# Kernel optimization log

Hardware: AMD Instinct MI355X
Metric: run time of the kernel (lower is better)

Reference implementation:

```python
import jax, jax.numpy as jnp
import numpy as np

THETA = 10000.0

def apply_rope(x, positions):
    # x: [B, H, S, d_k], positions: [S] int
    d_k = x.shape[-1]
    inv_freq = THETA ** (-jnp.arange(0, d_k, 2, dtype=jnp.float32) / d_k)  # [d_k/2]
    ang = positions.astype(jnp.float32)[:, None] * inv_freq[None, :]        # [S, d_k/2]
    cos, sin = jnp.cos(ang), jnp.sin(ang)
    x_even = x[..., 0::2]
    x_odd = x[..., 1::2]
    r_even = x_even * cos - x_odd * sin
    r_odd = x_even * sin + x_odd * cos
    # interleave back
    return jnp.stack([r_even, r_odd], axis=-1).reshape(x.shape)

def setup_inputs() -> dict:
    key = jax.random.key(0)
    k1, k2, k3 = jax.random.split(key, 3)
    B, S, D = 2, 2048, 1024
    x = jax.random.normal(k1, (B, S, D), dtype=jnp.float32)
    token_positions = jnp.arange(S, dtype=jnp.int32)
    W_qkv = jax.random.normal(k2, (3 * D, D), dtype=jnp.float32) * 0.02
    W_o = jax.random.normal(k3, (D, D), dtype=jnp.float32) * 0.02
    return {"x": x, "token_positions": token_positions, "W_qkv": W_qkv, "W_o": W_o}

def reference(x, token_positions, W_qkv, W_o):
    B, S, D = x.shape
    H = 16
    d_k = D // H
    qkv = jnp.einsum('bsd,ed->bse', x, W_qkv)           # [B, S, 3D]
    q, k, v = jnp.split(qkv, 3, axis=-1)
    def to_heads(t):
        return t.reshape(B, S, H, d_k).transpose(0, 2, 1, 3)  # [B, H, S, d_k]
    hq, hk, hv = to_heads(q), to_heads(k), to_heads(v)
    hq = apply_rope(hq, token_positions)
    hk = apply_rope(hk, token_positions)
    scale = d_k ** -0.5
    scores = jnp.einsum('bhqd,bhkd->bhqk', hq, hk) * scale  # [B, H, S, S]
    causal = jnp.tril(jnp.ones((S, S), dtype=bool))
    scores = jnp.where(causal, scores, -jnp.inf)
    attn = jax.nn.softmax(scores, axis=-1)
    out = jnp.einsum('bhqk,bhkd->bhqd', attn, hv)           # [B, H, S, d_k]
    out = out.transpose(0, 2, 1, 3).reshape(B, S, D)
    return jnp.einsum('bsd,ed->bse', out, W_o)
```

## Files before the change

### kernel.cpp

```cpp
#include <hip/hip_runtime.h>
#include <math.h>

typedef short short8 __attribute__((ext_vector_type(8)));
typedef float f32x4 __attribute__((ext_vector_type(4)));
typedef unsigned int u32x2 __attribute__((ext_vector_type(2)));

typedef __attribute__((address_space(1))) const void* as1p;
typedef __attribute__((address_space(3))) void* as3p;

__device__ __forceinline__ unsigned short f2bf(float f) {
    unsigned int u = __float_as_uint(f);
    u += 0x7fffu + ((u >> 16) & 1u);
    return (unsigned short)(u >> 16);
}

__global__ void cvt_all_bf16(const float* __restrict__ x,
                             const float* __restrict__ wqkv,
                             const float* __restrict__ wo,
                             unsigned short* __restrict__ xb,
                             unsigned short* __restrict__ wqkvb,
                             unsigned short* __restrict__ wob) {
    int i = blockIdx.x * blockDim.x + threadIdx.x;
    const float* src;
    unsigned short* dst;
    int off;
    if (i < 1048576)       { src = x;    dst = xb;    off = i; }
    else if (i < 1835008)  { src = wqkv; dst = wqkvb; off = i - 1048576; }
    else                   { src = wo;   dst = wob;   off = i - 1835008; }
    float4 v = ((const float4*)src)[off];
    ushort4 o = make_ushort4(f2bf(v.x), f2bf(v.y), f2bf(v.z), f2bf(v.w));
    ((ushort4*)dst)[off] = o;
}

template <int RF, int NTX, bool BF16_OUT, bool DO_ROPE>
__global__ __launch_bounds__(256) void gemm_nt_mfma(
    const unsigned short* __restrict__ A, const unsigned short* __restrict__ B,
    void* __restrict__ Cv, const int* __restrict__ pos, int N, int K) {
    constexpr int BM = RF * 32;
    __shared__ unsigned short As[BM * 32];
    __shared__ unsigned short Bs[128 * 32];
    const int tid = threadIdx.x;
    const int wave = tid >> 6, lane = tid & 63;
    const int L = blockIdx.x;
    const int xcd = L & 7, idx = L >> 3;
    const int nt_ = xcd * NTX + idx % NTX;
    const int mt  = idx / NTX;
    const int m0 = mt * BM, n0 = nt_ << 7;
    const int wr = ((wave >> 1) & 1) * (RF * 16);
    const int wc = (wave & 1) << 6;

    const int r0 = tid >> 2;
    const int ko = (((tid & 3) ^ ((r0 >> 1) & 3)) << 3);
    const unsigned short* Ap0 = A + (size_t)(m0 + r0) * K + ko;
    const unsigned short* Ap1 = A + (size_t)(m0 + (RF == 4 ? 64 : 0) + r0) * K + ko;
    const unsigned short* Bp0 = B + (size_t)(n0 + r0) * K + ko;
    const unsigned short* Bp1 = B + (size_t)(n0 + 64 + r0) * K + ko;

    f32x4 acc[RF][4] = {};
    const int lro = lane & 15;
    const int cs = ((lane >> 4) ^ ((lro >> 1) & 3)) << 3;

    for (int k0 = 0; k0 < K; k0 += 32) {
        __syncthreads();
        __builtin_amdgcn_global_load_lds((as1p)(Ap0 + k0), (as3p)(As + tid * 8), 16, 0, 0);
        if constexpr (RF == 4)
            __builtin_amdgcn_global_load_lds((as1p)(Ap1 + k0), (as3p)(As + (256 + tid) * 8), 16, 0, 0);
        __builtin_amdgcn_global_load_lds((as1p)(Bp0 + k0), (as3p)(Bs + tid * 8), 16, 0, 0);
        __builtin_amdgcn_global_load_lds((as1p)(Bp1 + k0), (as3p)(Bs + (256 + tid) * 8), 16, 0, 0);
        __syncthreads();

        short8 af[RF], bfr[4];
        #pragma unroll
        for (int i = 0; i < RF; i++) af[i] = *(const short8*)&As[(wr + i * 16 + lro) * 32 + cs];
        #pragma unroll
        for (int j = 0; j < 4; j++) bfr[j] = *(const short8*)&Bs[(wc + j * 16 + lro) * 32 + cs];
        #pragma unroll
        for (int i = 0; i < RF; i++)
            #pragma unroll
            for (int j = 0; j < 4; j++)
                acc[i][j] = __builtin_amdgcn_mfma_f32_16x16x32_bf16(af[i], bfr[j], acc[i][j], 0, 0, 0);
    }

    const int row_b = m0 + wr + ((lane >> 4) << 2);
    const int col_b = n0 + wc + lro;

    if constexpr (DO_ROPE) {
        const int sec = (n0 + wc) >> 10;
        if (sec < 2) {
            const float qs = (sec == 0) ? 0.18033688011112042f : 1.0f;
            const float sgn = (lane & 1) ? 1.0f : -1.0f;
            float ps[RF * 4];
            #pragma unroll
            for (int i = 0; i < RF; i++)
                #pragma unroll
                for (int r = 0; r < 4; r++)
                    ps[i * 4 + r] = (float)pos[(row_b + i * 16 + r) & 2047];
            #pragma unroll
            for (int j = 0; j < 4; j++) {
                float invf_rev = exp2f(-(float)((lro >> 1) + 8 * j) * 0.41524101186092029f)
                                 * 0.15915494309189535f;
                #pragma unroll
                for (int i = 0; i < RF; i++)
                    #pragma unroll
                    for (int r = 0; r < 4; r++) {
                        float rev = ps[i * 4 + r] * invf_rev;
                        rev -= floorf(rev);
                        float c = __builtin_amdgcn_cosf(rev) * qs;
                        float s = __builtin_amdgcn_sinf(rev) * (qs * sgn);
                        float mine = acc[i][j][r];
                        float partner = __shfl_xor(mine, 1, 64);
                        acc[i][j][r] = mine * c + partner * s;
                    }
            }
        }
    }

    #pragma unroll
    for (int i = 0; i < RF; i++)
        #pragma unroll
        for (int j = 0; j < 4; j++)
            #pragma unroll
            for (int r = 0; r < 4; r++) {
                size_t idx2 = (size_t)(row_b + i * 16 + r) * N + (col_b + j * 16);
                if constexpr (BF16_OUT) ((unsigned short*)Cv)[idx2] = f2bf(acc[i][j][r]);
                else ((float*)Cv)[idx2] = acc[i][j][r];
            }
}

__global__ __launch_bounds__(256) void flash_attn_mfma(
    const unsigned short* __restrict__ qkv, unsigned short* __restrict__ Ows) {
    const int S = 2048, D3 = 3072;
    const int L = blockIdx.x + (blockIdx.y << 4) + (blockIdx.z << 8);
    const int xcd = L & 7, t = L >> 3;
    const int pp = t & 15;
    const int g2 = xcd + ((t >> 4) << 3);
    const int h = g2 & 15, b = g2 >> 4;
    const int tid = threadIdx.x, wave = tid >> 6, lane = tid & 63;
    const int lro = lane & 15, grp = lane >> 4;

    __shared__ __align__(16) unsigned int Vp[2][64 * 35];
    __shared__ float RedW[4][16][66];
    __shared__ float Lbuf[4][4][16];

    const int m = tid >> 3;
    const int vo = (tid & 7) << 3;
    const int vcb = (wave << 3) + (grp << 1);
    const int klb = (wave << 4) + (grp << 2);

    const unsigned short* kbg = qkv + (size_t)(b * S) * D3 + 1024 + h * 64;
    const unsigned short* vbg = qkv + (size_t)(b * S) * D3 + 2048 + h * 64;

    const unsigned short* kfp = kbg + (size_t)(16 * wave + lro) * D3 + grp * 8;
    const unsigned short* vfp = vbg + (size_t)(2 * m) * D3 + vo;

    for (int ph = 0; ph < 2; ph++) {
        const int qt = ph ? 31 - pp : pp;
        const int q0 = qt << 6;
        const int nkt = qt + 1;

        __syncthreads();

        short8 bq[4][2];
        #pragma unroll
        for (int f = 0; f < 4; f++) {
            const unsigned short* qrow =
                qkv + (size_t)(b * S + q0 + f * 16 + lro) * D3 + h * 64 + grp * 8;
            bq[f][0] = *(const short8*)qrow;
            bq[f][1] = *(const short8*)(qrow + 32);
        }

        short8 kc0 = *(const short8*)kfp;
        short8 kc1 = *(const short8*)(kfp + 32);
        {
            uint4 va = *(const uint4*)vfp;
            uint4 vb = *(const uint4*)(vfp + D3);
            const unsigned short* pa_ = (const unsigned short*)&va;
            const unsigned short* pb_ = (const unsigned short*)&vb;
            #pragma unroll
            for (int j = 0; j < 8; j++)
                Vp[0][(vo + j) * 35 + m] = (unsigned)pa_[j] | ((unsigned)pb_[j] << 16);
        }
        __syncthreads();

        f32x4 acc[4][4] = {};
        float lsum[4] = {0.f, 0.f, 0.f, 0.f};

        for (int kt = 0; kt < nkt; kt++) {
            const int cur = kt & 1, nxt = cur ^ 1;
            const bool pf = (kt + 1 < nkt);
            short8 kn0, kn1;
            uint4 vna, vnb;
            if (pf) {
                const size_t off = (size_t)((kt + 1) * 64) * D3;
                kn0 = *(const short8*)(kfp + off);
                kn1 = *(const short8*)(kfp + off + 32);
                vna = *(const uint4*)(vfp + off);
                vnb = *(const uint4*)(vfp + off + D3);
            }

            f32x4 s0 = {}, s1 = {}, s2 = {}, s3 = {};
            s0 = __builtin_amdgcn_mfma_f32_16x16x32_bf16(kc0, bq[0][0], s0, 0, 0, 0);
            s0 = __builtin_amdgcn_mfma_f32_16x16x32_bf16(kc1, bq[0][1], s0, 0, 0, 0);
            s1 = __builtin_amdgcn_mfma_f32_16x16x32_bf16(kc0, bq[1][0], s1, 0, 0, 0);
            s1 = __builtin_amdgcn_mfma_f32_16x16x32_bf16(kc1, bq[1][1], s1, 0, 0, 0);
            s2 = __builtin_amdgcn_mfma_f32_16x16x32_bf16(kc0, bq[2][0], s2, 0, 0, 0);
            s2 = __builtin_amdgcn_mfma_f32_16x16x32_bf16(kc1, bq[2][1], s2, 0, 0, 0);
            s3 = __builtin_amdgcn_mfma_f32_16x16x32_bf16(kc0, bq[3][0], s3, 0, 0, 0);
            s3 = __builtin_amdgcn_mfma_f32_16x16x32_bf16(kc1, bq[3][1], s3, 0, 0, 0);
            f32x4 sf[4] = {s0, s1, s2, s3};

            const bool dg = (kt == nkt - 1);
            u32x2 pw[4];
            #pragma unroll
            for (int f = 0; f < 4; f++) {
                float v0 = sf[f][0], v1 = sf[f][1], v2 = sf[f][2], v3 = sf[f][3];
                if (dg) {
                    int thr = (f << 4) + lro - klb;
                    if (0 > thr) v0 = -1e30f;
                    if (1 > thr) v1 = -1e30f;
                    if (2 > thr) v2 = -1e30f;
                    if (3 > thr) v3 = -1e30f;
                }
                float p0 = __builtin_amdgcn_exp2f(v0);
                float p1 = __builtin_amdgcn_exp2f(v1);
                float p2 = __builtin_amdgcn_exp2f(v2);
                float p3 = __builtin_amdgcn_exp2f(v3);
                lsum[f] += (p0 + p1) + (p2 + p3);
                unsigned u0, u1;
                asm("v_cvt_pk_bf16_f32 %0, %1, %2" : "=v"(u0) : "v"(p0), "v"(p1));
                asm("v_cvt_pk_bf16_f32 %0, %1, %2" : "=v"(u1) : "v"(p2), "v"(p3));
                pw[f][0] = u0;
                pw[f][1] = u1;
            }

            u32x2 vv[4];
            #pragma unroll
            for (int nt = 0; nt < 4; nt++) {
                const unsigned* vr = &Vp[cur][(nt * 16 + lro) * 35 + vcb];
                vv[nt][0] = vr[0];
                vv[nt][1] = vr[1];
            }

            #pragma unroll
            for (int f = 0; f < 4; f++)
                #pragma unroll
                for (int nt = 0; nt < 4; nt++)
                    asm("v_mfma_f32_16x16x16_bf16 %0, %1, %2, %0"
                        : "+v"(acc[f][nt]) : "v"(pw[f]), "v"(vv[nt]));

            if (pf) {
                const unsigned short* pa_ = (const unsigned short*)&vna;
                const unsigned short* pb_ = (const unsigned short*)&vnb;
                #pragma unroll
                for (int j = 0; j < 8; j++)
                    Vp[nxt][(vo + j) * 35 + m] = (unsigned)pa_[j] | ((unsigned)pb_[j] << 16);
                kc0 = kn0;
                kc1 = kn1;
            }
            __syncthreads();
        }

        #pragma unroll
        for (int f = 0; f < 4; f++) {
            lsum[f] += __shfl_xor(lsum[f], 16, 64);
            lsum[f] += __shfl_xor(lsum[f], 32, 64);
        }
        if (lane < 16) {
            #pragma unroll
            for (int f = 0; f < 4; f++) Lbuf[wave][f][lro] = lsum[f];
        }

        #pragma unroll
        for (int f = 0; f < 4; f++) {
            __syncthreads();
            if (wave != f) {
                #pragma unroll
                for (int nt = 0; nt < 4; nt++)
                    #pragma unroll
                    for (int r = 0; r < 4; r++)
                        RedW[wave][(grp << 2) + r][nt * 16 + lro] = acc[f][nt][r];
            }
            __syncthreads();
            if (wave == f) {
                #pragma unroll
                for (int w2 = 0; w2 < 4; w2++) {
                    if (w2 == f) continue;
                    #pragma unroll
                    for (int nt = 0; nt < 4; nt++)
                        #pragma unroll
                        for (int r = 0; r < 4; r++)
                            acc[f][nt][r] += RedW[w2][(grp << 2) + r][nt * 16 + lro];
                }
                #pragma unroll
                for (int r = 0; r < 4; r++) {
                    int q = (grp << 2) + r;
                    float lt = Lbuf[0][f][q] + Lbuf[1][f][q] +
                               Lbuf[2][f][q] + Lbuf[3][f][q];
                    float inv = 1.0f / lt;
                    int row = q0 + (f << 4) + q;
                    #pragma unroll
                    for (int nt = 0; nt < 4; nt++)
                        Ows[(size_t)(b * S + row) * 1024 + h * 64 + nt * 16 + lro] =
                            f2bf(acc[f][nt][r] * inv);
                }
            }
        }
    }
}

extern "C" void kernel_launch(void* const* d_in, const int* in_sizes, int n_in,
                              void* d_out, int out_size, void* d_ws, size_t ws_size,
                              hipStream_t stream) {
    const float* x    = (const float*)d_in[0];
    const int*   pos  = (const int*)d_in[1];
    const float* Wqkv = (const float*)d_in[2];
    const float* Wo   = (const float*)d_in[3];
    float* out = (float*)d_out;

    unsigned short* xb    = (unsigned short*)d_ws;
    unsigned short* Wqkvb = xb + (size_t)4096 * 1024;
    unsigned short* Wob   = Wqkvb + (size_t)3072 * 1024;
    unsigned short* qkvb  = Wob + (size_t)1024 * 1024;
    unsigned short* Owsb  = qkvb + (size_t)4096 * 3072;

    cvt_all_bf16<<<8192, 256, 0, stream>>>(x, Wqkv, Wo, xb, Wqkvb, Wob);

    gemm_nt_mfma<4, 3, true, true><<<768, 256, 0, stream>>>(
        xb, Wqkvb, qkvb, pos, 3072, 1024);

    flash_attn_mfma<<<dim3(16, 16, 2), 256, 0, stream>>>(qkvb, Owsb);

    gemm_nt_mfma<2, 1, false, false><<<512, 256, 0, stream>>>(
        Owsb, Wob, out, nullptr, 1024, 1024);
}
```

Measured before the change: 180.2 us.

## Split flash-attention query rows across two wave groups using 512-thread blocks

Doubles the attention block from 4 to 8 waves. Each group of 4 waves now handles half of the 64 query rows, with the key columns still split four ways within the group, so the per-wave accumulator and score registers are halved. The aim is more waves in flight per block and lower register pressure, for better latency hiding. In exchange, K fragments are loaded twice per block (once per query group), only the first 256 threads stage V, and the cross-wave reduction now needs a larger shared-memory buffer.

```diff
diff --git a/kernel.cpp b/kernel.cpp
--- a/kernel.cpp
+++ b/kernel.cpp
@@ -127,7 +127,7 @@
             }
 }
 
-__global__ __launch_bounds__(256) void flash_attn_mfma(
+__global__ __launch_bounds__(512) void flash_attn_mfma(
     const unsigned short* __restrict__ qkv, unsigned short* __restrict__ Ows) {
     const int S = 2048, D3 = 3072;
     const int L = blockIdx.x + (blockIdx.y << 4) + (blockIdx.z << 8);
@@ -137,20 +137,21 @@
     const int h = g2 & 15, b = g2 >> 4;
     const int tid = threadIdx.x, wave = tid >> 6, lane = tid & 63;
     const int lro = lane & 15, grp = lane >> 4;
+    const int ks = wave & 3, qs = wave >> 2;
 
     __shared__ __align__(16) unsigned int Vp[2][64 * 35];
-    __shared__ float RedW[4][16][66];
-    __shared__ float Lbuf[4][4][16];
+    __shared__ float RedW[8][16][66];
+    __shared__ float Lbuf[8][2][16];
 
     const int m = tid >> 3;
     const int vo = (tid & 7) << 3;
-    const int vcb = (wave << 3) + (grp << 1);
-    const int klb = (wave << 4) + (grp << 2);
+    const int vcb = (ks << 3) + (grp << 1);
+    const int klb = (ks << 4) + (grp << 2);
 
     const unsigned short* kbg = qkv + (size_t)(b * S) * D3 + 1024 + h * 64;
     const unsigned short* vbg = qkv + (size_t)(b * S) * D3 + 2048 + h * 64;
 
-    const unsigned short* kfp = kbg + (size_t)(16 * wave + lro) * D3 + grp * 8;
+    const unsigned short* kfp = kbg + (size_t)(16 * ks + lro) * D3 + grp * 8;
     const unsigned short* vfp = vbg + (size_t)(2 * m) * D3 + vo;
 
     for (int ph = 0; ph < 2; ph++) {
@@ -160,18 +161,18 @@
 
         __syncthreads();
 
-        short8 bq[4][2];
-        #pragma unroll
-        for (int f = 0; f < 4; f++) {
+        short8 bq[2][2];
+        #pragma unroll
+        for (int i = 0; i < 2; i++) {
             const unsigned short* qrow =
-                qkv + (size_t)(b * S + q0 + f * 16 + lro) * D3 + h * 64 + grp * 8;
-            bq[f][0] = *(const short8*)qrow;
-            bq[f][1] = *(const short8*)(qrow + 32);
+                qkv + (size_t)(b * S + q0 + (2 * qs + i) * 16 + lro) * D3 + h * 64 + grp * 8;
+            bq[i][0] = *(const short8*)qrow;
+            bq[i][1] = *(const short8*)(qrow + 32);
         }
 
         short8 kc0 = *(const short8*)kfp;
         short8 kc1 = *(const short8*)(kfp + 32);
-        {
+        if (tid < 256) {
             uint4 va = *(const uint4*)vfp;
             uint4 vb = *(const uint4*)(vfp + D3);
             const unsigned short* pa_ = (const unsigned short*)&va;
@@ -182,8 +183,8 @@
         }
         __syncthreads();
 
-        f32x4 acc[4][4] = {};
-        float lsum[4] = {0.f, 0.f, 0.f, 0.f};
+        f32x4 acc[2][4] = {};
+        float lsum[2] = {0.f, 0.f};
 
         for (int kt = 0; kt < nkt; kt++) {
             const int cur = kt & 1, nxt = cur ^ 1;
@@ -194,28 +195,26 @@
                 const size_t off = (size_t)((kt + 1) * 64) * D3;
                 kn0 = *(const short8*)(kfp + off);
                 kn1 = *(const short8*)(kfp + off + 32);
-                vna = *(const uint4*)(vfp + off);
-                vnb = *(const uint4*)(vfp + off + D3);
-            }
-
-            f32x4 s0 = {}, s1 = {}, s2 = {}, s3 = {};
+                if (tid < 256) {
+                    vna = *(const uint4*)(vfp + off);
+                    vnb = *(const uint4*)(vfp + off + D3);
+                }
+            }
+
+            f32x4 s0 = {}, s1 = {};
             s0 = __builtin_amdgcn_mfma_f32_16x16x32_bf16(kc0, bq[0][0], s0, 0, 0, 0);
             s0 = __builtin_amdgcn_mfma_f32_16x16x32_bf16(kc1, bq[0][1], s0, 0, 0, 0);
             s1 = __builtin_amdgcn_mfma_f32_16x16x32_bf16(kc0, bq[1][0], s1, 0, 0, 0);
             s1 = __builtin_amdgcn_mfma_f32_16x16x32_bf16(kc1, bq[1][1], s1, 0, 0, 0);
-            s2 = __builtin_amdgcn_mfma_f32_16x16x32_bf16(kc0, bq[2][0], s2, 0, 0, 0);
-            s2 = __builtin_amdgcn_mfma_f32_16x16x32_bf16(kc1, bq[2][1], s2, 0, 0, 0);
-            s3 = __builtin_amdgcn_mfma_f32_16x16x32_bf16(kc0, bq[3][0], s3, 0, 0, 0);
-            s3 = __builtin_amdgcn_mfma_f32_16x16x32_bf16(kc1, bq[3][1], s3, 0, 0, 0);
-            f32x4 sf[4] = {s0, s1, s2, s3};
+            f32x4 sf[2] = {s0, s1};
 
             const bool dg = (kt == nkt - 1);
-            u32x2 pw[4];
-            #pragma unroll
-            for (int f = 0; f < 4; f++) {
-                float v0 = sf[f][0], v1 = sf[f][1], v2 = sf[f][2], v3 = sf[f][3];
+            u32x2 pw[2];
+            #pragma unroll
+            for (int i = 0; i < 2; i++) {
+                float v0 = sf[i][0], v1 = sf[i][1], v2 = sf[i][2], v3 = sf[i][3];
                 if (dg) {
-                    int thr = (f << 4) + lro - klb;
+                    int thr = ((2 * qs + i) << 4) + lro - klb;
                     if (0 > thr) v0 = -1e30f;
                     if (1 > thr) v1 = -1e30f;
                     if (2 > thr) v2 = -1e30f;
@@ -225,12 +224,12 @@
                 float p1 = __builtin_amdgcn_exp2f(v1);
                 float p2 = __builtin_amdgcn_exp2f(v2);
                 float p3 = __builtin_amdgcn_exp2f(v3);
-                lsum[f] += (p0 + p1) + (p2 + p3);
+                lsum[i] += (p0 + p1) + (p2 + p3);
                 unsigned u0, u1;
                 asm("v_cvt_pk_bf16_f32 %0, %1, %2" : "=v"(u0) : "v"(p0), "v"(p1));
                 asm("v_cvt_pk_bf16_f32 %0, %1, %2" : "=v"(u1) : "v"(p2), "v"(p3));
-                pw[f][0] = u0;
-                pw[f][1] = u1;
+                pw[i][0] = u0;
+                pw[i][1] = u1;
             }
 
             u32x2 vv[4];
@@ -242,18 +241,20 @@
             }
 
             #pragma unroll
-            for (int f = 0; f < 4; f++)
+            for (int i = 0; i < 2; i++)
                 #pragma unroll
                 for (int nt = 0; nt < 4; nt++)
                     asm("v_mfma_f32_16x16x16_bf16 %0, %1, %2, %0"
-                        : "+v"(acc[f][nt]) : "v"(pw[f]), "v"(vv[nt]));
+                        : "+v"(acc[i][nt]) : "v"(pw[i]), "v"(vv[nt]));
 
             if (pf) {
-                const unsigned short* pa_ = (const unsigned short*)&vna;
-                const unsigned short* pb_ = (const unsigned short*)&vnb;
-                #pragma unroll
-                for (int j = 0; j < 8; j++)
-                    Vp[nxt][(vo + j) * 35 + m] = (unsigned)pa_[j] | ((unsigned)pb_[j] << 16);
+                if (tid < 256) {
+                    const unsigned short* pa_ = (const unsigned short*)&vna;
+                    const unsigned short* pb_ = (const unsigned short*)&vnb;
+                    #pragma unroll
+                    for (int j = 0; j < 8; j++)
+                        Vp[nxt][(vo + j) * 35 + m] = (unsigned)pa_[j] | ((unsigned)pb_[j] << 16);
+                }
                 kc0 = kn0;
                 kc1 = kn1;
             }
@@ -261,47 +262,45 @@
         }
 
         #pragma unroll
-        for (int f = 0; f < 4; f++) {
-            lsum[f] += __shfl_xor(lsum[f], 16, 64);
-            lsum[f] += __shfl_xor(lsum[f], 32, 64);
+        for (int i = 0; i < 2; i++) {
+            lsum[i] += __shfl_xor(lsum[i], 16, 64);
+            lsum[i] += __shfl_xor(lsum[i], 32, 64);
         }
         if (lane < 16) {
-            #pragma unroll
-            for (int f = 0; f < 4; f++) Lbuf[wave][f][lro] = lsum[f];
-        }
-
-        #pragma unroll
-        for (int f = 0; f < 4; f++) {
+            Lbuf[wave][0][lro] = lsum[0];
+            Lbuf[wave][1][lro] = lsum[1];
+        }
+
+        #pragma unroll
+        for (int fi = 0; fi < 2; fi++) {
             __syncthreads();
-            if (wave != f) {
+            if (ks != 0) {
                 #pragma unroll
                 for (int nt = 0; nt < 4; nt++)
                     #pragma unroll
                     for (int r = 0; r < 4; r++)
-                        RedW[wave][(grp << 2) + r][nt * 16 + lro] = acc[f][nt][r];
+                        RedW[wave][(grp << 2) + r][nt * 16 + lro] = acc[fi][nt][r];
             }
             __syncthreads();
-            if (wave == f) {
-                #pragma unroll
-                for (int w2 = 0; w2 < 4; w2++) {
-                    if (w2 == f) continue;
+            if (ks == 0) {
+                #pragma unroll
+                for (int j = 1; j < 4; j++)
                     #pragma unroll
                     for (int nt = 0; nt < 4; nt++)
                         #pragma unroll
                         for (int r = 0; r < 4; r++)
-                            acc[f][nt][r] += RedW[w2][(grp << 2) + r][nt * 16 + lro];
-                }
+                            acc[fi][nt][r] += RedW[(qs << 2) + j][(grp << 2) + r][nt * 16 + lro];
                 #pragma unroll
                 for (int r = 0; r < 4; r++) {
                     int q = (grp << 2) + r;
-                    float lt = Lbuf[0][f][q] + Lbuf[1][f][q] +
-                               Lbuf[2][f][q] + Lbuf[3][f][q];
+                    float lt = Lbuf[(qs << 2) + 0][fi][q] + Lbuf[(qs << 2) + 1][fi][q] +
+                               Lbuf[(qs << 2) + 2][fi][q] + Lbuf[(qs << 2) + 3][fi][q];
                     float inv = 1.0f / lt;
-                    int row = q0 + (f << 4) + q;
+                    int row = q0 + ((2 * qs + fi) << 4) + q;
                     #pragma unroll
                     for (int nt = 0; nt < 4; nt++)
                         Ows[(size_t)(b * S + row) * 1024 + h * 64 + nt * 16 + lro] =
-                            f2bf(acc[f][nt][r] * inv);
+                            f2bf(acc[fi][nt][r] * inv);
                 }
             }
         }
@@ -328,7 +327,7 @@
     gemm_nt_mfma<4, 3, true, true><<<768, 256, 0, stream>>>(
         xb, Wqkvb, qkvb, pos, 3072, 1024);
 
-    flash_attn_mfma<<<dim3(16, 16, 2), 256, 0, stream>>>(qkvb, Owsb);
+    flash_attn_mfma<<<dim3(16, 16, 2), 512, 0, stream>>>(qkvb, Owsb);
 
     gemm_nt_mfma<2, 1, false, false><<<512, 256, 0, stream>>>(
         Owsb, Wob, out, nullptr, 1024, 1024);
```

After: 187.6 us. 4.1% more time.
